# Kernel optimization log

Measured on AMD Instinct MI355X. Metric: run time of the kernel, lower is better.

Reference implementation:

```python
import jax, jax.numpy as jnp
import numpy as np

# dims: L layers, D d_model, H heads, DH head_dim, DFF ffn, V vocab, BLK nf4 blocksize
L, D, H, DH, DFF, V, BLK = 2, 2048, 16, 128, 5504, 32000, 64
B, S, C, T = 4, 1000, 7, 45

# bitsandbytes NF4 codebook (fixed 16 quantiles of N(0,1), normalized to [-1,1])
NF4 = jnp.array([-1.0, -0.6961928009986877, -0.5250730514526367, -0.39491748809814453,
                 -0.28444138169288635, -0.18477343022823334, -0.09105003625154495, 0.0,
                 0.07958029955625534, 0.16093020141124725, 0.24611230194568634,
                 0.3379152417182922, 0.44070982933044434, 0.5626170039176941,
                 0.7229568362236023, 1.0], dtype=jnp.float32)


def _dequant(idx, scale):
    # idx: [out, in] int in [0,16); scale: [out, in//BLK] per-block absmax
    o, i = idx.shape
    return (NF4[idx].reshape(o, i // BLK, BLK) * scale[:, :, None]).reshape(o, i)


def _rmsnorm(h, w, eps=1e-5):
    return h * jax.lax.rsqrt(jnp.mean(h * h, axis=-1, keepdims=True) + eps) * w


def _rot_half(x):
    x1, x2 = jnp.split(x, 2, axis=-1)
    return jnp.concatenate([-x2, x1], axis=-1)


def _llama_fwd(token_ids, embed, wq_idx, wq_scale, wk_idx, wk_scale, wv_idx, wv_scale,
               wo_idx, wo_scale, wg_idx, wg_scale, wu_idx, wu_scale, wd_idx, wd_scale,
               ln1_w, ln2_w, lnf_w):
    Bt, St = token_ids.shape
    h = embed[token_ids]  # [B,S,D]
    # rotary embeddings
    inv = 1.0 / (10000.0 ** (jnp.arange(0, DH, 2, dtype=jnp.float32) / DH))
    ang = jnp.arange(St, dtype=jnp.float32)[:, None] * inv[None, :]  # [S, DH/2]
    emb_ang = jnp.concatenate([ang, ang], axis=-1)  # [S, DH]
    cos, sin = jnp.cos(emb_ang), jnp.sin(emb_ang)
    mask = jnp.where(jnp.tril(jnp.ones((St, St), dtype=bool)), 0.0, -1e9)  # causal
    for l in range(L):
        xn = _rmsnorm(h, ln1_w[l])
        q = (xn @ _dequant(wq_idx[l], wq_scale[l]).T).reshape(Bt, St, H, DH).transpose(0, 2, 1, 3)
        k = (xn @ _dequant(wk_idx[l], wk_scale[l]).T).reshape(Bt, St, H, DH).transpose(0, 2, 1, 3)
        v = (xn @ _dequant(wv_idx[l], wv_scale[l]).T).reshape(Bt, St, H, DH).transpose(0, 2, 1, 3)
        q = q * cos + _rot_half(q) * sin
        k = k * cos + _rot_half(k) * sin
        att = jax.nn.softmax(jnp.einsum('bhqd,bhkd->bhqk', q, k) / np.float32(np.sqrt(DH)) + mask, axis=-1)
        ctx = jnp.einsum('bhqk,bhkd->bhqd', att, v).transpose(0, 2, 1, 3).reshape(Bt, St, D)
        h = h + ctx @ _dequant(wo_idx[l], wo_scale[l]).T
        xn = _rmsnorm(h, ln2_w[l])
        g = xn @ _dequant(wg_idx[l], wg_scale[l]).T
        u = xn @ _dequant(wu_idx[l], wu_scale[l]).T
        h = h + (jax.nn.silu(g) * u) @ _dequant(wd_idx[l], wd_scale[l]).T
    # hidden_states[-1].mean(dim=1)
    return _rmsnorm(h, lnf_w).mean(axis=1)


def setup_inputs() -> dict:
    key = jax.random.key(0)
    ks = jax.random.split(key, 20)
    ridx = lambda k, shp: jax.random.randint(k, shp, 0, 16, dtype=jnp.int32)
    rsc = lambda k, shp: jax.random.uniform(k, shp, minval=0.01, maxval=0.03, dtype=jnp.float32)
    return {
        'x': jax.random.normal(ks[0], (B, C, T), dtype=jnp.float32),
        'token_ids': jax.random.randint(ks[1], (B, S), 0, V, dtype=jnp.int32),
        'embed': jax.random.normal(ks[2], (V, D), dtype=jnp.float32) * 0.02,
        'wq_idx': ridx(ks[3], (L, D, D)), 'wq_scale': rsc(ks[4], (L, D, D // BLK)),
        'wk_idx': ridx(ks[5], (L, D, D)), 'wk_scale': rsc(ks[6], (L, D, D // BLK)),
        'wv_idx': ridx(ks[7], (L, D, D)), 'wv_scale': rsc(ks[8], (L, D, D // BLK)),
        'wo_idx': ridx(ks[9], (L, D, D)), 'wo_scale': rsc(ks[10], (L, D, D // BLK)),
        'wg_idx': ridx(ks[11], (L, DFF, D)), 'wg_scale': rsc(ks[12], (L, DFF, D // BLK)),
        'wu_idx': ridx(ks[13], (L, DFF, D)), 'wu_scale': rsc(ks[14], (L, DFF, D // BLK)),
        'wd_idx': ridx(ks[15], (L, D, DFF)), 'wd_scale': rsc(ks[16], (L, D, DFF // BLK)),
        'ln1_w': jnp.ones((L, D), dtype=jnp.float32),
        'ln2_w': jnp.ones((L, D), dtype=jnp.float32),
        'lnf_w': jnp.ones((D,), dtype=jnp.float32),
        'proj_w': jax.random.normal(ks[17], (D, T), dtype=jnp.float32) * 0.05,
        'proj_b': jnp.zeros((D,), dtype=jnp.float32),
    }


def reference(x, token_ids, embed, wq_idx, wq_scale, wk_idx, wk_scale, wv_idx, wv_scale,
              wo_idx, wo_scale, wg_idx, wg_scale, wu_idx, wu_scale, wd_idx, wd_scale,
              ln1_w, ln2_w, lnf_w, proj_w, proj_b):
    # NF4-quantized Llama-style causal LM forward + mean pool over sequence
    e_text = _llama_fwd(token_ids, embed, wq_idx, wq_scale, wk_idx, wk_scale, wv_idx, wv_scale,
                        wo_idx, wo_scale, wg_idx, wg_scale, wu_idx, wu_scale, wd_idx, wd_scale,
                        ln1_w, ln2_w, lnf_w)  # [B, D]
    # series branch: channel-mean -> linear -> L2 normalize
    series_mean = x.mean(axis=1)  # [B, T]
    series_emb = series_mean @ proj_w.T + proj_b  # [B, D]
    series_emb = series_emb / jnp.maximum(jnp.linalg.norm(series_emb, axis=-1, keepdims=True), 1e-12)
    return e_text + series_emb
```

## Files before the change

### kernel.cpp

```cpp
#include <hip/hip_runtime.h>
#include <hip/hip_bf16.h>

#define L_N 2
#define D_ 2048
#define H_ 16
#define DH_ 128
#define DFF_ 5504
#define B_ 4
#define S_ 1000
#define C_ 7
#define T_ 45
#define M_ 4000

typedef short bf16x8 __attribute__((ext_vector_type(8)));
typedef float f32x4 __attribute__((ext_vector_type(4)));

__constant__ float NF4_TAB[16] = {
  -1.0f, -0.6961928009986877f, -0.5250730514526367f, -0.39491748809814453f,
  -0.28444138169288635f, -0.18477343022823334f, -0.09105003625154495f, 0.0f,
  0.07958029955625534f, 0.16093020141124725f, 0.24611230194568634f,
  0.3379152417182922f, 0.44070982933044434f, 0.5626170039176941f,
  0.7229568362236023f, 1.0f };

__device__ __forceinline__ unsigned short f2bf(float f) {
  unsigned int u = __float_as_uint(f);
  u += 0x7fffu + ((u >> 16) & 1u);
  return (unsigned short)(u >> 16);
}
__device__ __forceinline__ float bf2f(unsigned short u) {
  return __uint_as_float(((unsigned int)u) << 16);
}
__device__ __forceinline__ f32x4 zero4() { f32x4 z; z[0]=0.f; z[1]=0.f; z[2]=0.f; z[3]=0.f; return z; }
__device__ __forceinline__ f32x4 mfma16(bf16x8 a, bf16x8 b, f32x4 c) {
  return __builtin_amdgcn_mfma_f32_16x16x32_bf16(a, b, c, 0, 0, 0);
}

typedef __attribute__((address_space(3))) unsigned int lds_u32;
typedef const __attribute__((address_space(1))) unsigned int glb_u32;
__device__ __forceinline__ void gload16(const void* g, void* l) {
  __builtin_amdgcn_global_load_lds((glb_u32*)g, (lds_u32*)l, 16, 0, 0);
}

__global__ void rope_tables(float* __restrict__ cosT, float* __restrict__ sinT) {
  int s = blockIdx.x, d = threadIdx.x;
  int j = d & 63;
  float inv = expf(-(float)j * (9.210340371976184f / 64.f));
  float ang = (float)s * inv;
  cosT[s * DH_ + d] = cosf(ang);
  sinT[s * DH_ + d] = sinf(ang);
}

__global__ __launch_bounds__(256) void embed_gather(const int* __restrict__ tok,
    const float* __restrict__ emb, float* __restrict__ h) {
  int row = blockIdx.x;
  int tk = tok[row];
  const float4* src = reinterpret_cast<const float4*>(emb + (size_t)tk * D_);
  float4* dst = reinterpret_cast<float4*>(h + (size_t)row * D_);
  dst[threadIdx.x] = src[threadIdx.x];
  dst[threadIdx.x + 256] = src[threadIdx.x + 256];
}

__global__ __launch_bounds__(256) void rmsnorm_k(const float* __restrict__ h,
    const float* __restrict__ w, unsigned short* __restrict__ out) {
  const int row = blockIdx.x, t = threadIdx.x;
  const float* hp = h + (size_t)row * D_;
  float4 a = *reinterpret_cast<const float4*>(&hp[t * 8]);
  float4 b = *reinterpret_cast<const float4*>(&hp[t * 8 + 4]);
  float ss = a.x*a.x + a.y*a.y + a.z*a.z + a.w*a.w
           + b.x*b.x + b.y*b.y + b.z*b.z + b.w*b.w;
#pragma unroll
  for (int m = 1; m < 64; m <<= 1) ss += __shfl_xor(ss, m);
  __shared__ float red[4];
  if ((t & 63) == 0) red[t >> 6] = ss;
  __syncthreads();
  float tot = red[0] + red[1] + red[2] + red[3];
  float rs = rsqrtf(tot * (1.0f / D_) + 1e-5f);
  float4 wa = *reinterpret_cast<const float4*>(&w[t * 8]);
  float4 wb = *reinterpret_cast<const float4*>(&w[t * 8 + 4]);
  unsigned r0 = (unsigned)f2bf(a.x*rs*wa.x) | ((unsigned)f2bf(a.y*rs*wa.y) << 16);
  unsigned r1 = (unsigned)f2bf(a.z*rs*wa.z) | ((unsigned)f2bf(a.w*rs*wa.w) << 16);
  unsigned r2 = (unsigned)f2bf(b.x*rs*wb.x) | ((unsigned)f2bf(b.y*rs*wb.y) << 16);
  unsigned r3 = (unsigned)f2bf(b.z*rs*wb.z) | ((unsigned)f2bf(b.w*rs*wb.w) << 16);
  int4 ov; ov.x = (int)r0; ov.y = (int)r1; ov.z = (int)r2; ov.w = (int)r3;
  *reinterpret_cast<int4*>(&out[(size_t)row * D_ + t * 8]) = ov;
}

struct DqJob { const int* idx; const float* sc; unsigned short* out; };
struct DqBatch { DqJob j[4]; };

__global__ __launch_bounds__(256) void dequant_batch(DqBatch bt, int K) {
  __shared__ float nf4[16];
  const int t = threadIdx.x;
  if (t < 16) nf4[t] = NF4_TAB[t];
  __syncthreads();
  const DqJob jb = bt.j[blockIdx.z];
  const int row = blockIdx.y;
  const int k0 = blockIdx.x * 2048 + t * 8;
  if (k0 >= K) return;
  const size_t base = (size_t)row * K + k0;
  int4 a = *reinterpret_cast<const int4*>(&jb.idx[base]);
  int4 b = *reinterpret_cast<const int4*>(&jb.idx[base + 4]);
  float s = jb.sc[(size_t)row * (K >> 6) + (k0 >> 6)];
  unsigned r0 = (unsigned)f2bf(nf4[a.x & 15] * s) | ((unsigned)f2bf(nf4[a.y & 15] * s) << 16);
  unsigned r1 = (unsigned)f2bf(nf4[a.z & 15] * s) | ((unsigned)f2bf(nf4[a.w & 15] * s) << 16);
  unsigned r2 = (unsigned)f2bf(nf4[b.x & 15] * s) | ((unsigned)f2bf(nf4[b.y & 15] * s) << 16);
  unsigned r3 = (unsigned)f2bf(nf4[b.z & 15] * s) | ((unsigned)f2bf(nf4[b.w & 15] * s) << 16);
  int4 ov; ov.x = (int)r0; ov.y = (int)r1; ov.z = (int)r2; ov.w = (int)r3;
  *reinterpret_cast<int4*>(&jb.out[base]) = ov;
}

template<int MODE, int DBUF>
__global__ __launch_bounds__(256) void gemm_bf16(
    const unsigned short* __restrict__ A,
    const unsigned short* __restrict__ Bw,
    int Mdim, int N, int K, int nx,
    void* outp, const unsigned short* gin) {
  __shared__ unsigned short A_lds[(DBUF + 1) * 128 * 64];
  __shared__ unsigned short B_lds[(DBUF + 1) * 128 * 64];
  const int t = threadIdx.x;
  const int lane = t & 63, wid = t >> 6;

  const int nwg = gridDim.x;
  const int bid = blockIdx.x;
  const int wg = (bid & 7) * (nwg >> 3) + (bid >> 3);
  const int n0 = (wg % nx) * 128;
  const int m0 = (wg / nx) * 128;

  const int wm = (wid >> 1) * 64, wn = (wid & 1) * 64;
  const int lr = lane & 15, lg = lane >> 4;
  const int lrow = lane >> 3;
  const int lslot = (((lane & 7) ^ lrow) << 4);
  const int rswz = (lr & 7) << 4;

  f32x4 acc[4][4];
#pragma unroll
  for (int i = 0; i < 4; ++i)
#pragma unroll
    for (int j = 0; j < 4; ++j) acc[i][j] = zero4();

  const int kT = K >> 6;
  const size_t rowb = (size_t)(K * 2);

  auto stage = [&](int kt, int b) {
#pragma unroll
    for (int c0 = 0; c0 < 4; ++c0) {
      const int c = wid + 4 * c0;
      int gr = m0 + c * 8 + lrow;
      gr = gr < Mdim ? gr : Mdim - 1;
      gload16((const char*)A + (size_t)gr * rowb + kt * 128 + lslot,
              (char*)&A_lds[0] + b * 16384 + c * 1024);
      const int nr = n0 + c * 8 + lrow;
      gload16((const char*)Bw + (size_t)nr * rowb + kt * 128 + lslot,
              (char*)&B_lds[0] + b * 16384 + c * 1024);
    }
  };
  auto compute = [&](int cur) {
#pragma unroll
    for (int ks = 0; ks < 2; ++ks) {
      bf16x8 af[4], bfr[4];
      const int cb = (ks * 64 + lg * 16) ^ rswz;
#pragma unroll
      for (int i = 0; i < 4; ++i) {
        af[i]  = *reinterpret_cast<const bf16x8*>(
                   (const char*)&A_lds[0] + cur * 16384 + (wm + i * 16 + lr) * 128 + cb);
        bfr[i] = *reinterpret_cast<const bf16x8*>(
                   (const char*)&B_lds[0] + cur * 16384 + (wn + i * 16 + lr) * 128 + cb);
      }
      __builtin_amdgcn_s_setprio(1);
#pragma unroll
      for (int mi = 0; mi < 4; ++mi)
#pragma unroll
        for (int ni = 0; ni < 4; ++ni)
          acc[mi][ni] = mfma16(af[mi], bfr[ni], acc[mi][ni]);
      __builtin_amdgcn_s_setprio(0);
    }
  };

  if (DBUF) {
    stage(0, 0);
    __syncthreads();
    for (int kt = 0; kt < kT; ++kt) {
      const int cur = kt & 1;
      if (kt + 1 < kT) stage(kt + 1, cur ^ 1);
      compute(cur);
      __syncthreads();
    }
  } else {
    for (int kt = 0; kt < kT; ++kt) {
      stage(kt, 0);
      __syncthreads();
      compute(0);
      __syncthreads();
    }
  }

#pragma unroll
  for (int mi = 0; mi < 4; ++mi) {
#pragma unroll
    for (int r = 0; r < 4; ++r) {
      int gm = m0 + wm + mi * 16 + lg * 4 + r;
      if (gm >= Mdim) continue;
#pragma unroll
      for (int ni = 0; ni < 4; ++ni) {
        int gn = n0 + wn + ni * 16 + lr;
        float v = acc[mi][ni][r];
        if (MODE == 0) {
          ((unsigned short*)outp)[(size_t)gm * N + gn] = f2bf(v);
        } else if (MODE == 1) {
          const int which = gn >> 11;
          const int hh = (gn >> 7) & 15, dd = gn & 127;
          const int b = gm / S_, s = gm - b * S_;
          ((unsigned short*)outp)[
            (((size_t)which * (B_ * H_) + b * H_ + hh) * S_ + s) * DH_ + dd] = f2bf(v);
        } else if (MODE == 2) {
          float g = bf2f(gin[(size_t)gm * N + gn]);
          float sg = g / (1.f + __expf(-g));
          ((unsigned short*)outp)[(size_t)gm * N + gn] = f2bf(sg * v);
        } else {
          ((float*)outp)[(size_t)gm * N + gn] += v;
        }
      }
    }
  }
}

__global__ __launch_bounds__(256) void rope_apply(unsigned short* __restrict__ qb,
    unsigned short* __restrict__ kb, const float* __restrict__ cosT,
    const float* __restrict__ sinT) {
  size_t i = (size_t)blockIdx.x * 256 + threadIdx.x;
  int d = (int)(i & 63);
  size_t row = i >> 6;
  int s = (int)(row % S_);
  size_t base = row * DH_;
  float c = cosT[s * DH_ + d], sn = sinT[s * DH_ + d];
  float q0 = bf2f(qb[base + d]), q1 = bf2f(qb[base + d + 64]);
  qb[base + d]      = f2bf(q0 * c - q1 * sn);
  qb[base + d + 64] = f2bf(q1 * c + q0 * sn);
  float k0 = bf2f(kb[base + d]), k1 = bf2f(kb[base + d + 64]);
  kb[base + d]      = f2bf(k0 * c - k1 * sn);
  kb[base + d + 64] = f2bf(k1 * c + k0 * sn);
}

__global__ __launch_bounds__(256) void vtrans_k(const unsigned short* __restrict__ vb,
    unsigned short* __restrict__ vt) {
  __shared__ unsigned int tile[64][33];
  const int t = threadIdx.x;
  const int s0 = blockIdx.x * 64, d0 = blockIdx.y * 64, bh = blockIdx.z;
#pragma unroll
  for (int j = 0; j < 2; ++j) {
    int idx = t + 256 * j;
    int s_r = idx >> 3, c8 = (idx & 7) << 3;
    int srow = s0 + s_r; srow = srow < S_ ? srow : S_ - 1;
    int4 v = *reinterpret_cast<const int4*>(&vb[((size_t)bh * S_ + srow) * DH_ + d0 + c8]);
    tile[s_r][(c8 >> 1) + 0] = (unsigned)v.x;
    tile[s_r][(c8 >> 1) + 1] = (unsigned)v.y;
    tile[s_r][(c8 >> 1) + 2] = (unsigned)v.z;
    tile[s_r][(c8 >> 1) + 3] = (unsigned)v.w;
  }
  __syncthreads();
#pragma unroll
  for (int j = 0; j < 2; ++j) {
    int idx = t + 256 * j;
    int d_r = idx >> 3, s8 = (idx & 7) << 3;
    unsigned r[8];
#pragma unroll
    for (int e = 0; e < 8; ++e) {
      unsigned wv = tile[s8 + e][d_r >> 1];
      r[e] = (d_r & 1) ? (wv >> 16) : (wv & 0xffffu);
    }
    int4 ov;
    ov.x = (int)(r[0] | (r[1] << 16));
    ov.y = (int)(r[2] | (r[3] << 16));
    ov.z = (int)(r[4] | (r[5] << 16));
    ov.w = (int)(r[6] | (r[7] << 16));
    *reinterpret_cast<int4*>(&vt[((size_t)(bh * 128 + d0 + d_r)) * 1024 + s0 + s8]) = ov;
  }
}

__global__ __launch_bounds__(512, 4) void attn2_k(const unsigned short* __restrict__ qg,
    const unsigned short* __restrict__ kg, const unsigned short* __restrict__ vtg,
    unsigned short* __restrict__ ctx) {
  __shared__ unsigned short K_lds[64 * 128];
  __shared__ unsigned short VT_lds[128 * 64];
  const int t = threadIdx.x, lane = t & 63, w = t >> 6;
  const int lr = lane & 15, lg = lane >> 4;
  const int bh = blockIdx.x, qt = blockIdx.y;
  const int q0 = qt * 128;
  const int b = bh >> 4, hh = bh & 15;
  const size_t kbase2 = (size_t)bh * S_ * DH_ * 2;
  const int q_idx = q0 + w * 16 + lr;
  const int swz = (lr & 7) << 4;

  bf16x8 qf[4];
#pragma unroll
  for (int ks = 0; ks < 4; ++ks) {
    bf16x8 z;
#pragma unroll
    for (int e = 0; e < 8; ++e) z[e] = 0;
    if (q_idx < S_)
      z = *reinterpret_cast<const bf16x8*>(
            (const char*)qg + kbase2 + (size_t)q_idx * 256 + ks * 64 + lg * 16);
    qf[ks] = z;
  }
  float mst = -1e30f, lst = 0.f;
  f32x4 cacc[8];
#pragma unroll
  for (int f = 0; f < 8; ++f) cacc[f] = zero4();

  const int q_hi = (q0 + 127 < S_) ? q0 + 127 : S_ - 1;
  const int nt = q_hi / 64 + 1;
  const int wq_max = q0 + w * 16 + 15;

  for (int kt = 0; kt < nt; ++kt) {
    const int kv0 = kt * 64;
    __syncthreads();
#pragma unroll
    for (int j = 0; j < 2; ++j) {
      const int chunk = w + 8 * j;
      int krow = chunk * 4 + (lane >> 4);
      int kcolb = (lane & 15) << 4;
      int gr = kv0 + krow; gr = gr < S_ ? gr : S_ - 1;
      gload16((const char*)kg + kbase2 + (size_t)gr * 256 + (kcolb ^ ((krow & 7) << 4)),
              (char*)K_lds + chunk * 1024);
      int vrow = chunk * 8 + (lane >> 3);
      int vcolb = (lane & 7) << 4;
      gload16((const char*)vtg + ((size_t)(bh * 128 + vrow) * 1024 + kv0) * 2 + (vcolb ^ ((vrow & 7) << 4)),
              (char*)VT_lds + chunk * 1024);
    }
    __syncthreads();
    if (kv0 > wq_max) continue;

    f32x4 sacc[4];
#pragma unroll
    for (int c = 0; c < 4; ++c) sacc[c] = zero4();
#pragma unroll
    for (int ks = 0; ks < 4; ++ks) {
#pragma unroll
      for (int c = 0; c < 4; ++c) {
        bf16x8 kf = *reinterpret_cast<const bf16x8*>(
            &K_lds[(c * 16 + lr) * 128 + (((ks * 64 + lg * 16) ^ swz) >> 1)]);
        sacc[c] = mfma16(kf, qf[ks], sacc[c]);
      }
    }
    float p[4][4];
    float mx = -1e30f;
#pragma unroll
    for (int c = 0; c < 4; ++c)
#pragma unroll
      for (int r = 0; r < 4; ++r) {
        int kv = kv0 + c * 16 + lg * 4 + r;
        float v = sacc[c][r] * 0.08838834764831845f;
        if (kv > q_idx || kv >= S_) v = -1e30f;
        p[c][r] = v;
        mx = fmaxf(mx, v);
      }
    mx = fmaxf(mx, __shfl_xor(mx, 16));
    mx = fmaxf(mx, __shfl_xor(mx, 32));
    float mn = fmaxf(mst, mx);
    float corr = __expf(mst - mn);
    mst = mn;
    float rs = 0.f;
#pragma unroll
    for (int c = 0; c < 4; ++c)
#pragma unroll
      for (int r = 0; r < 4; ++r) {
        float e = __expf(p[c][r] - mn);
        p[c][r] = e;
        rs += e;
      }
    rs += __shfl_xor(rs, 16);
    rs += __shfl_xor(rs, 32);
    lst = lst * corr + rs;
#pragma unroll
    for (int f = 0; f < 8; ++f)
#pragma unroll
      for (int r = 0; r < 4; ++r) cacc[f][r] *= corr;

    unsigned pk01[4], pk23[4];
#pragma unroll
    for (int c = 0; c < 4; ++c) {
      pk01[c] = (unsigned)f2bf(p[c][0]) | ((unsigned)f2bf(p[c][1]) << 16);
      pk23[c] = (unsigned)f2bf(p[c][2]) | ((unsigned)f2bf(p[c][3]) << 16);
    }
#pragma unroll
    for (int ks = 0; ks < 2; ++ks) {
      unsigned bu[4];
#pragma unroll
      for (int jj = 0; jj < 4; ++jj) {
        const int srcl = ((lg & 1) * 2 + (jj >> 1)) * 16 + lr;
        unsigned lo = (unsigned)__shfl((int)((jj & 1) ? pk23[2 * ks]     : pk01[2 * ks]),     srcl);
        unsigned hi = (unsigned)__shfl((int)((jj & 1) ? pk23[2 * ks + 1] : pk01[2 * ks + 1]), srcl);
        bu[jj] = (lg >= 2) ? hi : lo;
      }
      union { unsigned u[4]; bf16x8 v; } pb;
      pb.u[0] = bu[0]; pb.u[1] = bu[1]; pb.u[2] = bu[2]; pb.u[3] = bu[3];
#pragma unroll
      for (int f = 0; f < 8; ++f) {
        bf16x8 vtf = *reinterpret_cast<const bf16x8*>(
            &VT_lds[(f * 16 + lr) * 64 + (((ks * 64 + lg * 16) ^ swz) >> 1)]);
        cacc[f] = mfma16(vtf, pb.v, cacc[f]);
      }
    }
  }

  if (q_idx < S_) {
    float inv = 1.f / lst;
    unsigned short* cp = ctx + ((size_t)(b * S_ + q_idx)) * D_ + hh * 128;
#pragma unroll
    for (int f = 0; f < 8; ++f) {
      unsigned lo = (unsigned)f2bf(cacc[f][0] * inv) | ((unsigned)f2bf(cacc[f][1] * inv) << 16);
      unsigned hi = (unsigned)f2bf(cacc[f][2] * inv) | ((unsigned)f2bf(cacc[f][3] * inv) << 16);
      uint2 ov; ov.x = lo; ov.y = hi;
      *reinterpret_cast<uint2*>(cp + f * 16 + lg * 4) = ov;
    }
  }
}

__global__ __launch_bounds__(256) void meanpool(const unsigned short* __restrict__ xn,
    float* __restrict__ out) {
  int d = blockIdx.x * 256 + threadIdx.x;
  int b = blockIdx.y;
  const unsigned short* p = xn + (size_t)b * S_ * D_ + d;
  float s = 0.f;
  for (int i = 0; i < S_; ++i) s += bf2f(p[(size_t)i * D_]);
  out[(size_t)b * D_ + d] = s * (1.f / S_);
}

__global__ __launch_bounds__(256) void series_k(const float* __restrict__ x,
    const float* __restrict__ pw, const float* __restrict__ pb, float* out) {
  __shared__ float sm[T_];
  __shared__ float emb[D_];
  __shared__ float red[4];
  int b = blockIdx.x, t = threadIdx.x;
  if (t < T_) {
    float s = 0.f;
    for (int c = 0; c < C_; ++c) s += x[((size_t)b * C_ + c) * T_ + t];
    sm[t] = s * (1.f / C_);
  }
  __syncthreads();
  float ssq = 0.f;
#pragma unroll
  for (int j = 0; j < D_ / 256; ++j) {
    int d = j * 256 + t;
    float e = pb[d];
    for (int tt = 0; tt < T_; ++tt) e += sm[tt] * pw[(size_t)d * T_ + tt];
    emb[d] = e;
    ssq += e * e;
  }
#pragma unroll
  for (int m = 1; m < 64; m <<= 1) ssq += __shfl_xor(ssq, m);
  if ((t & 63) == 0) red[t >> 6] = ssq;
  __syncthreads();
  float tot = red[0] + red[1] + red[2] + red[3];
  float inv = 1.f / fmaxf(sqrtf(tot), 1e-12f);
#pragma unroll
  for (int j = 0; j < D_ / 256; ++j) {
    int d = j * 256 + t;
    out[(size_t)b * D_ + d] += emb[d] * inv;
  }
}

extern "C" void kernel_launch(void* const* d_in, const int* in_sizes, int n_in,
                              void* d_out, int out_size, void* d_ws, size_t ws_size,
                              hipStream_t stream) {
  const float* x      = (const float*)d_in[0];
  const int*   tok    = (const int*)d_in[1];
  const float* embedw = (const float*)d_in[2];
  const int*   wq_idx = (const int*)d_in[3];
  const float* wq_sc  = (const float*)d_in[4];
  const int*   wk_idx = (const int*)d_in[5];
  const float* wk_sc  = (const float*)d_in[6];
  const int*   wv_idx = (const int*)d_in[7];
  const float* wv_sc  = (const float*)d_in[8];
  const int*   wo_idx = (const int*)d_in[9];
  const float* wo_sc  = (const float*)d_in[10];
  const int*   wg_idx = (const int*)d_in[11];
  const float* wg_sc  = (const float*)d_in[12];
  const int*   wu_idx = (const int*)d_in[13];
  const float* wu_sc  = (const float*)d_in[14];
  const int*   wd_idx = (const int*)d_in[15];
  const float* wd_sc  = (const float*)d_in[16];
  const float* ln1    = (const float*)d_in[17];
  const float* ln2    = (const float*)d_in[18];
  const float* lnf    = (const float*)d_in[19];
  const float* projw  = (const float*)d_in[20];
  const float* projb  = (const float*)d_in[21];
  float* out = (float*)d_out;
  (void)in_sizes; (void)n_in; (void)out_size; (void)ws_size;

  char* wsp = (char*)d_ws;
  size_t off = 0;
  auto alloc = [&](size_t bytes) -> void* {
    void* p = wsp + off; off += (bytes + 255) & ~(size_t)255; return p; };
  float* cosT = (float*)alloc((size_t)S_ * DH_ * 4);
  float* sinT = (float*)alloc((size_t)S_ * DH_ * 4);
  float* hbuf = (float*)alloc((size_t)M_ * D_ * 4);
  unsigned short* xn   = (unsigned short*)alloc((size_t)M_ * D_ * 2);
  unsigned short* qkv  = (unsigned short*)alloc((size_t)3 * B_ * H_ * S_ * DH_ * 2);
  unsigned short* wdeq = (unsigned short*)alloc((size_t)2 * DFF_ * D_ * 2);
  unsigned short* vt   = (unsigned short*)alloc((size_t)B_ * H_ * DH_ * 1024 * 2);
  const size_t NH = (size_t)B_ * H_ * S_ * DH_;
  unsigned short* qb = qkv, *kb = qkv + NH, *vb = qkv + 2 * NH;
  unsigned short* ctx  = xn;
  unsigned short* gbuf = qkv;

  rope_tables<<<S_, DH_, 0, stream>>>(cosT, sinT);
  embed_gather<<<M_, 256, 0, stream>>>(tok, embedw, hbuf);

  const int my = (M_ + 127) / 128;
  const dim3 gQKV((3 * D_ / 128) * my);
  const dim3 gAtt((D_ / 128) * my);
  const dim3 gMlp((DFF_ / 128) * my);
  const size_t DD = (size_t)D_ * D_;
  const size_t FD = (size_t)DFF_ * D_;

  for (int l = 0; l < L_N; ++l) {
    const int*   wqi = wq_idx + (size_t)l * DD;
    const float* wqs = wq_sc + (size_t)l * D_ * (D_ / 64);
    const int*   wki = wk_idx + (size_t)l * DD;
    const float* wks = wk_sc + (size_t)l * D_ * (D_ / 64);
    const int*   wvi = wv_idx + (size_t)l * DD;
    const float* wvs = wv_sc + (size_t)l * D_ * (D_ / 64);
    const int*   woi = wo_idx + (size_t)l * DD;
    const float* wos = wo_sc + (size_t)l * D_ * (D_ / 64);
    const int*   wgi = wg_idx + (size_t)l * FD;
    const float* wgs = wg_sc + (size_t)l * DFF_ * (D_ / 64);
    const int*   wui = wu_idx + (size_t)l * FD;
    const float* wus = wu_sc + (size_t)l * DFF_ * (D_ / 64);
    const int*   wdi = wd_idx + (size_t)l * FD;
    const float* wds = wd_sc + (size_t)l * D_ * (DFF_ / 64);

    rmsnorm_k<<<M_, 256, 0, stream>>>(hbuf, ln1 + l * D_, xn);

    {
      DqBatch bt;
      bt.j[0] = { wqi, wqs, wdeq };
      bt.j[1] = { wki, wks, wdeq + DD };
      bt.j[2] = { wvi, wvs, wdeq + 2 * DD };
      bt.j[3] = { woi, wos, wdeq + 3 * DD };
      dequant_batch<<<dim3(1, D_, 4), 256, 0, stream>>>(bt, D_);
    }
    gemm_bf16<1, 1><<<gQKV, 256, 0, stream>>>(xn, wdeq, M_, 3 * D_, D_, 3 * D_ / 128,
                                              qkv, nullptr);
    rope_apply<<<(B_ * H_ * S_ * 64) / 256, 256, 0, stream>>>(qb, kb, cosT, sinT);
    vtrans_k<<<dim3(16, 2, B_ * H_), 256, 0, stream>>>(vb, vt);
    attn2_k<<<dim3(B_ * H_, 8), 512, 0, stream>>>(qb, kb, vt, ctx);
    gemm_bf16<3, 1><<<gAtt, 256, 0, stream>>>(ctx, wdeq + 3 * DD, M_, D_, D_, D_ / 128,
                                              hbuf, nullptr);
    rmsnorm_k<<<M_, 256, 0, stream>>>(hbuf, ln2 + l * D_, xn);

    {
      DqBatch bt;
      bt.j[0] = { wgi, wgs, wdeq };
      bt.j[1] = { wui, wus, wdeq + FD };
      bt.j[2] = bt.j[0]; bt.j[3] = bt.j[0];
      dequant_batch<<<dim3(1, DFF_, 2), 256, 0, stream>>>(bt, D_);
    }
    gemm_bf16<0, 0><<<gMlp, 256, 0, stream>>>(xn, wdeq, M_, DFF_, D_, DFF_ / 128,
                                              gbuf, nullptr);
    gemm_bf16<2, 1><<<gMlp, 256, 0, stream>>>(xn, wdeq + FD, M_, DFF_, D_, DFF_ / 128,
                                              gbuf, gbuf);

    {
      DqBatch bt;
      bt.j[0] = { wdi, wds, wdeq };
      bt.j[1] = bt.j[0]; bt.j[2] = bt.j[0]; bt.j[3] = bt.j[0];
      dequant_batch<<<dim3(3, D_, 1), 256, 0, stream>>>(bt, DFF_);
    }
    gemm_bf16<3, 1><<<gAtt, 256, 0, stream>>>(gbuf, wdeq, M_, D_, DFF_, D_ / 128,
                                              hbuf, nullptr);
  }

  rmsnorm_k<<<M_, 256, 0, stream>>>(hbuf, lnf, xn);
  meanpool<<<dim3(D_ / 256, B_), 256, 0, stream>>>(xn, out);
  series_k<<<B_, 256, 0, stream>>>(x, projw, projb, out);
}
```

Measured before the change: 1.462 ms.

## Drop LDS double buffering for higher occupancy and add grouped tile mapping

Every GEMM now uses a single LDS buffer for A and B, which halves shared memory per block, and declares launch bounds of 256 threads with 5 blocks per CU. The aim is to hide global-load latency by running more resident workgroups instead of software double buffering. The gate GEMM also gets a grouped block-to-tile mapping that puts consecutive M tiles on the same XCD, for better L2 reuse of the weight tiles. In exchange, loads and MFMA work inside one block no longer overlap, and the register cap from the launch bounds could cause spills.

```diff
diff --git a/kernel.cpp b/kernel.cpp
--- a/kernel.cpp
+++ b/kernel.cpp
@@ -109,22 +109,31 @@
   *reinterpret_cast<int4*>(&jb.out[base]) = ov;
 }
 
-template<int MODE, int DBUF>
-__global__ __launch_bounds__(256) void gemm_bf16(
+template<int MODE, int GROUPED>
+__global__ __launch_bounds__(256, 5) void gemm_bf16(
     const unsigned short* __restrict__ A,
     const unsigned short* __restrict__ Bw,
     int Mdim, int N, int K, int nx,
     void* outp, const unsigned short* gin) {
-  __shared__ unsigned short A_lds[(DBUF + 1) * 128 * 64];
-  __shared__ unsigned short B_lds[(DBUF + 1) * 128 * 64];
+  __shared__ unsigned short A_lds[128 * 64];
+  __shared__ unsigned short B_lds[128 * 64];
   const int t = threadIdx.x;
   const int lane = t & 63, wid = t >> 6;
 
-  const int nwg = gridDim.x;
+  int m_blk, n_blk;
   const int bid = blockIdx.x;
-  const int wg = (bid & 7) * (nwg >> 3) + (bid >> 3);
-  const int n0 = (wg % nx) * 128;
-  const int m0 = (wg / nx) * 128;
+  if (GROUPED) {
+    const int xcd = bid & 7, l = bid >> 3;
+    m_blk = xcd * 4 + (l & 3);
+    n_blk = l >> 2;
+  } else {
+    const int nwg = gridDim.x;
+    const int wg = (bid & 7) * (nwg >> 3) + (bid >> 3);
+    n_blk = wg % nx;
+    m_blk = wg / nx;
+  }
+  const int n0 = n_blk * 128;
+  const int m0 = m_blk * 128;
 
   const int wm = (wid >> 1) * 64, wn = (wid & 1) * 64;
   const int lr = lane & 15, lg = lane >> 4;
@@ -141,20 +150,19 @@
   const int kT = K >> 6;
   const size_t rowb = (size_t)(K * 2);
 
-  auto stage = [&](int kt, int b) {
+  for (int kt = 0; kt < kT; ++kt) {
 #pragma unroll
     for (int c0 = 0; c0 < 4; ++c0) {
       const int c = wid + 4 * c0;
       int gr = m0 + c * 8 + lrow;
       gr = gr < Mdim ? gr : Mdim - 1;
       gload16((const char*)A + (size_t)gr * rowb + kt * 128 + lslot,
-              (char*)&A_lds[0] + b * 16384 + c * 1024);
+              (char*)&A_lds[0] + c * 1024);
       const int nr = n0 + c * 8 + lrow;
       gload16((const char*)Bw + (size_t)nr * rowb + kt * 128 + lslot,
-              (char*)&B_lds[0] + b * 16384 + c * 1024);
-    }
-  };
-  auto compute = [&](int cur) {
+              (char*)&B_lds[0] + c * 1024);
+    }
+    __syncthreads();
 #pragma unroll
     for (int ks = 0; ks < 2; ++ks) {
       bf16x8 af[4], bfr[4];
@@ -162,9 +170,9 @@
 #pragma unroll
       for (int i = 0; i < 4; ++i) {
         af[i]  = *reinterpret_cast<const bf16x8*>(
-                   (const char*)&A_lds[0] + cur * 16384 + (wm + i * 16 + lr) * 128 + cb);
+                   (const char*)&A_lds[0] + (wm + i * 16 + lr) * 128 + cb);
         bfr[i] = *reinterpret_cast<const bf16x8*>(
-                   (const char*)&B_lds[0] + cur * 16384 + (wn + i * 16 + lr) * 128 + cb);
+                   (const char*)&B_lds[0] + (wn + i * 16 + lr) * 128 + cb);
       }
       __builtin_amdgcn_s_setprio(1);
 #pragma unroll
@@ -174,24 +182,7 @@
           acc[mi][ni] = mfma16(af[mi], bfr[ni], acc[mi][ni]);
       __builtin_amdgcn_s_setprio(0);
     }
-  };
-
-  if (DBUF) {
-    stage(0, 0);
     __syncthreads();
-    for (int kt = 0; kt < kT; ++kt) {
-      const int cur = kt & 1;
-      if (kt + 1 < kT) stage(kt + 1, cur ^ 1);
-      compute(cur);
-      __syncthreads();
-    }
-  } else {
-    for (int kt = 0; kt < kT; ++kt) {
-      stage(kt, 0);
-      __syncthreads();
-      compute(0);
-      __syncthreads();
-    }
   }
 
 #pragma unroll
@@ -556,9 +547,9 @@
       bt.j[2] = bt.j[0]; bt.j[3] = bt.j[0];
       dequant_batch<<<dim3(1, DFF_, 2), 256, 0, stream>>>(bt, D_);
     }
-    gemm_bf16<0, 0><<<gMlp, 256, 0, stream>>>(xn, wdeq, M_, DFF_, D_, DFF_ / 128,
+    gemm_bf16<0, 1><<<gMlp, 256, 0, stream>>>(xn, wdeq, M_, DFF_, D_, DFF_ / 128,
                                               gbuf, nullptr);
-    gemm_bf16<2, 1><<<gMlp, 256, 0, stream>>>(xn, wdeq + FD, M_, DFF_, D_, DFF_ / 128,
+    gemm_bf16<2, 0><<<gMlp, 256, 0, stream>>>(xn, wdeq + FD, M_, DFF_, D_, DFF_ / 128,
                                               gbuf, gbuf);
 
     {
```

Measured after the change: 5.100 ms. +248.8%, slower.
